# Optimization experiments

Hardware: AMD Instinct MI355X
Metric: run time of the kernel (lower is better)

The kernel has to match this reference:

```python
import jax, jax.numpy as jnp
import numpy as np

N = 8192       # nodes per graph
E = 262144     # edges per graph (avg degree 32)
D_IN, D_H, D_OUT = 128, 256, 64


def _gcn_layer(x, src, dst, W, b, n):
    # PyG GCNConv: add self-loops, symmetric normalization D^-1/2 (A+I) D^-1/2, then + bias
    xw = x @ W
    loop = jnp.arange(n)
    src_f = jnp.concatenate([src, loop])
    dst_f = jnp.concatenate([dst, loop])
    deg = jax.ops.segment_sum(jnp.ones(src_f.shape[0], x.dtype), dst_f, num_segments=n)
    dinv = jax.lax.rsqrt(jnp.maximum(deg, jnp.asarray(1e-12, x.dtype)))
    norm = dinv[src_f] * dinv[dst_f]                      # [E+N]
    msg = xw[src_f] * norm[:, None]                       # gather + scale
    return jax.ops.segment_sum(msg, dst_f, num_segments=n) + b


def _cross_attn(x1, x2, q, k, v):
    Q = x1 @ q
    V = x1 @ v
    K = x2 @ k
    e = jax.nn.leaky_relu(Q @ K.T, negative_slope=0.01)  # [N1, N2]
    attn = jax.nn.softmax(e, axis=-1)
    return attn @ V


def setup_inputs() -> dict:
    key = jax.random.key(0)
    ks = jax.random.split(key, 20)
    std = 1.0 / np.sqrt(D_OUT)

    def gw(k, shape, fan_in):
        return jax.random.normal(k, shape, jnp.float32) * (1.0 / np.sqrt(fan_in))

    def uw(k, shape):
        return jax.random.uniform(k, shape, jnp.float32, -std, std)

    inp = {
        'graph_set1': jax.random.randint(ks[0], (2, E), 0, N),
        'graph_set2': jax.random.randint(ks[1], (2, E), 0, N),
        'x_set1': jax.random.normal(ks[2], (N, D_IN), jnp.float32),
        'x_set2': jax.random.normal(ks[3], (N, D_IN), jnp.float32),
        'W11': gw(ks[4], (D_IN, D_H), D_IN),  'b11': jnp.zeros((D_H,), jnp.float32),
        'W12': gw(ks[5], (D_H, D_OUT), D_H),  'b12': jnp.zeros((D_OUT,), jnp.float32),
        'W21': gw(ks[6], (D_IN, D_H), D_IN),  'b21': jnp.zeros((D_H,), jnp.float32),
        'W22': gw(ks[7], (D_H, D_OUT), D_H),  'b22': jnp.zeros((D_OUT,), jnp.float32),
        'q1': uw(ks[8], (D_OUT, D_OUT)), 'k1': uw(ks[9], (D_OUT, D_OUT)), 'v1': uw(ks[10], (D_OUT, D_OUT)),
        'q2': uw(ks[11], (D_OUT, D_OUT)), 'k2': uw(ks[12], (D_OUT, D_OUT)), 'v2': uw(ks[13], (D_OUT, D_OUT)),
    }
    return inp


def reference(graph_set1, graph_set2, x_set1, x_set2,
              W11, b11, W12, b12, W21, b21, W22, b22,
              q1, k1, v1, q2, k2, v2):
    s1, d1 = graph_set1[0], graph_set1[1]
    s2, d2 = graph_set2[0], graph_set2[1]
    # GCN branch 1
    h1 = jax.nn.relu(_gcn_layer(x_set1, s1, d1, W11, b11, N))
    h1 = _gcn_layer(h1, s1, d1, W12, b12, N)
    # GCN branch 2
    h2 = jax.nn.relu(_gcn_layer(x_set2, s2, d2, W21, b21, N))
    h2 = _gcn_layer(h2, s2, d2, W22, b22, N)
    # cross attention fusion (note cross2 consumes the updated out_set1)
    o1 = _cross_attn(h1, h2, q1, k1, v1)
    o2 = _cross_attn(h2, o1, q2, k2, v2)
    logits = (o1 @ o2.T).ravel()                          # [N*N]
    return logits
```

## Files before the change

kernel.cpp:

```cpp
#include <hip/hip_runtime.h>
#include <math.h>

static constexpr int NN = 8192;
static constexpr int NE = 262144;
static constexpr int NCH = 8;
static constexpr int NS = (NN / NCH) / 32;

typedef short bfrag __attribute__((ext_vector_type(8)));
typedef float f32x4 __attribute__((ext_vector_type(4)));

#define MFMA(a, b, c) __builtin_amdgcn_mfma_f32_16x16x32_bf16((a), (b), (c), 0, 0, 0)

__device__ __forceinline__ unsigned short f2bf(float x) {
  union { float f; unsigned u; } v; v.f = x;
  unsigned r = v.u + 0x7fffu + ((v.u >> 16) & 1u);
  return (unsigned short)(r >> 16);
}
__device__ __forceinline__ float bf2f(unsigned short h) {
  union { unsigned u; float f; } v; v.u = ((unsigned)h) << 16;
  return v.f;
}

__device__ __forceinline__ void gll16(const void* g, void* l) {
  __builtin_amdgcn_global_load_lds(
      (const __attribute__((address_space(1))) unsigned*)g,
      (__attribute__((address_space(3))) unsigned*)l, 16, 0, 0);
}


__global__ void k_count2(const int* __restrict__ d1, const int* __restrict__ d2,
                         int* __restrict__ i1, int* __restrict__ i2) {
  int t = blockIdx.x * 256 + threadIdx.x;
  const int* d = blockIdx.y ? d2 : d1;
  int* ii = blockIdx.y ? i2 : i1;
  if (t < NE) atomicAdd(&ii[d[t]], 1);
}

__global__ void k_scan2(const int* __restrict__ ideg1, int* __restrict__ off1,
                        int* __restrict__ cur1, float* __restrict__ dinv1,
                        const int* __restrict__ ideg2, int* __restrict__ off2,
                        int* __restrict__ cur2, float* __restrict__ dinv2) {
  const int* indeg = blockIdx.x ? ideg2 : ideg1;
  int* off = blockIdx.x ? off2 : off1;
  int* cur = blockIdx.x ? cur2 : cur1;
  float* dinv = blockIdx.x ? dinv2 : dinv1;
  __shared__ int sh[1024];
  __shared__ int carry;
  int t = threadIdx.x;
  if (t == 0) carry = 0;
  __syncthreads();
  for (int base = 0; base < NN; base += 1024) {
    int v = indeg[base + t];
    sh[t] = v;
    __syncthreads();
    for (int s = 1; s < 1024; s <<= 1) {
      int add = (t >= s) ? sh[t - s] : 0;
      __syncthreads();
      sh[t] += add;
      __syncthreads();
    }
    int excl = carry + sh[t] - v;
    off[base + t] = excl;
    cur[base + t] = excl;
    dinv[base + t] = 1.0f / sqrtf((float)(v + 1));
    __syncthreads();
    if (t == 1023) carry += sh[t];
    __syncthreads();
  }
  if (t == 0) off[NN] = carry;
}

__global__ void k_fill2(const int* __restrict__ s1, const int* __restrict__ d1,
                        int* __restrict__ c1, int* __restrict__ l1,
                        const int* __restrict__ s2, const int* __restrict__ d2,
                        int* __restrict__ c2, int* __restrict__ l2) {
  int t = blockIdx.x * 256 + threadIdx.x;
  const int* src = blockIdx.y ? s2 : s1;
  const int* dst = blockIdx.y ? d2 : d1;
  int* cur = blockIdx.y ? c2 : c1;
  int* out = blockIdx.y ? l2 : l1;
  if (t < NE) {
    int d = dst[t];
    int slot = atomicAdd(&cur[d], 1);
    out[slot] = src[t];
  }
}


__global__ void k_split_w(const float* W11, const float* W21, const float* W12,
                          const float* W22, const float* q1, const float* k1,
                          const float* v1, const float* q2, const float* k2,
                          const float* v2, short* __restrict__ whi,
                          short* __restrict__ wlo) {
  int y = blockIdx.y;
  const float* src; int R, C, base;
  if (y == 0)      { src = W11; R = 128; C = 256; base = 0; }
  else if (y == 1) { src = W21; R = 128; C = 256; base = 32768; }
  else if (y == 2) { src = W12; R = 256; C = 64;  base = 65536; }
  else if (y == 3) { src = W22; R = 256; C = 64;  base = 81920; }
  else if (y == 4) { src = q1;  R = 64;  C = 64;  base = 98304; }
  else if (y == 5) { src = k1;  R = 64;  C = 64;  base = 102400; }
  else if (y == 6) { src = v1;  R = 64;  C = 64;  base = 106496; }
  else if (y == 7) { src = q2;  R = 64;  C = 64;  base = 110592; }
  else if (y == 8) { src = k2;  R = 64;  C = 64;  base = 114688; }
  else             { src = v2;  R = 64;  C = 64;  base = 118784; }
  int idx = blockIdx.x * 256 + threadIdx.x;
  if (idx >= R * C) return;
  int r = idx / C, c = idx % C;
  float x = src[idx];
  unsigned short h = f2bf(x);
  whi[base + c * R + r] = (short)h;
  wlo[base + c * R + r] = (short)f2bf(x - bf2f(h));
}


__global__ __launch_bounds__(256) void k_agg1d(
    const float* __restrict__ x1, const float* __restrict__ x2,
    const int* __restrict__ off1, const int* __restrict__ srcl1,
    const float* __restrict__ dinv1, const int* __restrict__ off2,
    const int* __restrict__ srcl2, const float* __restrict__ dinv2,
    short* __restrict__ a1hi, short* __restrict__ a1lo,
    short* __restrict__ a2hi, short* __restrict__ a2lo) {
  int br = blockIdx.y;
  const float* x = br ? x2 : x1;
  const int* off = br ? off2 : off1;
  const int* srcl = br ? srcl2 : srcl1;
  const float* dinv = br ? dinv2 : dinv1;
  short* ahi = br ? a2hi : a1hi;
  short* alo = br ? a2lo : a1lo;
  int wave = threadIdx.x >> 6, lane = threadIdx.x & 63;
  int node = blockIdx.x * 4 + wave;
  float dn = dinv[node];
  const float2* xr = (const float2*)x;
  float ax, ay;
  { float2 v = xr[(size_t)node * 64 + lane]; ax = dn * v.x; ay = dn * v.y; }
  int p = off[node], e = off[node + 1];
  for (; p + 3 < e; p += 4) {
    int s0 = srcl[p], s1 = srcl[p + 1], s2 = srcl[p + 2], s3 = srcl[p + 3];
    float w0 = dinv[s0], w1 = dinv[s1], w2 = dinv[s2], w3 = dinv[s3];
    float2 v0 = xr[(size_t)s0 * 64 + lane], v1 = xr[(size_t)s1 * 64 + lane];
    float2 v2 = xr[(size_t)s2 * 64 + lane], v3 = xr[(size_t)s3 * 64 + lane];
    ax += w0 * v0.x + w1 * v1.x + w2 * v2.x + w3 * v3.x;
    ay += w0 * v0.y + w1 * v1.y + w2 * v2.y + w3 * v3.y;
  }
  for (; p < e; ++p) {
    int s = srcl[p];
    float w = dinv[s];
    float2 v = xr[(size_t)s * 64 + lane];
    ax += w * v.x; ay += w * v.y;
  }
  float ox = dn * ax, oy = dn * ay;
  unsigned short hx = f2bf(ox), hy = f2bf(oy);
  int o = node * 128 + lane * 2;
  *(short2*)(ahi + o) = make_short2((short)hx, (short)hy);
  *(short2*)(alo + o) = make_short2((short)f2bf(ox - bf2f(hx)),
                                    (short)f2bf(oy - bf2f(hy)));
}


__global__ __launch_bounds__(256) void k_agg2d(
    const float* __restrict__ t1, const float* __restrict__ t2,
    const int* __restrict__ off1, const int* __restrict__ srcl1,
    const float* __restrict__ dinv1, const int* __restrict__ off2,
    const int* __restrict__ srcl2, const float* __restrict__ dinv2,
    const float* __restrict__ b12, const float* __restrict__ b22,
    short* __restrict__ g1hi, short* __restrict__ g1lo,
    short* __restrict__ g2hi, short* __restrict__ g2lo) {
  int br = blockIdx.y;
  const float* t = br ? t2 : t1;
  const int* off = br ? off2 : off1;
  const int* srcl = br ? srcl2 : srcl1;
  const float* dinv = br ? dinv2 : dinv1;
  const float* bias = br ? b22 : b12;
  short* ghi = br ? g2hi : g1hi;
  short* glo = br ? g2lo : g1lo;
  int wave = threadIdx.x >> 6, lane = threadIdx.x & 63;
  int node = blockIdx.x * 4 + wave;
  float dn = dinv[node];
  float acc = dn * t[(size_t)node * 64 + lane];
  int p = off[node], e = off[node + 1];
  for (; p + 3 < e; p += 4) {
    int s0 = srcl[p], s1 = srcl[p + 1], s2 = srcl[p + 2], s3 = srcl[p + 3];
    float w0 = dinv[s0], w1 = dinv[s1], w2 = dinv[s2], w3 = dinv[s3];
    acc += w0 * t[(size_t)s0 * 64 + lane] + w1 * t[(size_t)s1 * 64 + lane] +
           w2 * t[(size_t)s2 * 64 + lane] + w3 * t[(size_t)s3 * 64 + lane];
  }
  for (; p < e; ++p) {
    int s = srcl[p];
    acc += dinv[s] * t[(size_t)s * 64 + lane];
  }
  float o = dn * acc + bias[lane];
  unsigned short h = f2bf(o);
  ghi[(size_t)node * 64 + lane] = (short)h;
  glo[(size_t)node * 64 + lane] = (short)f2bf(o - bf2f(h));
}


__global__ __launch_bounds__(64) void k_gemmL1(
    const short* __restrict__ a1hi, const short* __restrict__ a1lo,
    const short* __restrict__ a2hi, const short* __restrict__ a2lo,
    const short* __restrict__ whi, const short* __restrict__ wlo,
    const float* __restrict__ b11, const float* __restrict__ b21,
    short* __restrict__ h1hi, short* __restrict__ h1lo,
    short* __restrict__ h2hi, short* __restrict__ h2lo) {
  int br = blockIdx.z;
  const short* Ahi = br ? a2hi : a1hi;
  const short* Alo = br ? a2lo : a1lo;
  const short* Bh = whi + (br ? 32768 : 0);
  const short* Bl = wlo + (br ? 32768 : 0);
  const float* bias = br ? b21 : b11;
  short* Chi = br ? h2hi : h1hi;
  short* Clo = br ? h2lo : h1lo;
  int lane = threadIdx.x;
  int lo16 = lane & 15, hi4 = lane >> 4;
  int r0 = blockIdx.x * 16;
  int c0 = blockIdx.y * 64;
  bfrag ah[4], al[4];
  const char* abh = (const char*)Ahi + ((size_t)(r0 + lo16) * 128 + hi4 * 8) * 2;
  const char* abl = (const char*)Alo + ((size_t)(r0 + lo16) * 128 + hi4 * 8) * 2;
#pragma unroll
  for (int ks = 0; ks < 4; ++ks) {
    ah[ks] = *(const bfrag*)(abh + ks * 64);
    al[ks] = *(const bfrag*)(abl + ks * 64);
  }
  f32x4 z = {0.f, 0.f, 0.f, 0.f};
  f32x4 acc[4] = {z, z, z, z};
#pragma unroll
  for (int c = 0; c < 4; ++c) {
    const char* bbh = (const char*)Bh + ((size_t)(c0 + c * 16 + lo16) * 128 + hi4 * 8) * 2;
    const char* bbl = (const char*)Bl + ((size_t)(c0 + c * 16 + lo16) * 128 + hi4 * 8) * 2;
#pragma unroll
    for (int ks = 0; ks < 4; ++ks) {
      bfrag bh = *(const bfrag*)(bbh + ks * 64);
      bfrag bl = *(const bfrag*)(bbl + ks * 64);
      acc[c] = MFMA(ah[ks], bh, acc[c]);
      acc[c] = MFMA(ah[ks], bl, acc[c]);
      acc[c] = MFMA(al[ks], bh, acc[c]);
    }
  }
#pragma unroll
  for (int c = 0; c < 4; ++c) {
    int col = c0 + c * 16 + lo16;
    float bv = bias[col];
#pragma unroll
    for (int r = 0; r < 4; ++r) {
      int row = r0 + hi4 * 4 + r;
      float v = fmaxf(acc[c][r] + bv, 0.f);
      unsigned short h = f2bf(v);
      Chi[(size_t)row * 256 + col] = (short)h;
      Clo[(size_t)row * 256 + col] = (short)f2bf(v - bf2f(h));
    }
  }
}


__global__ __launch_bounds__(64) void k_gemmL2(
    const short* __restrict__ h1hi, const short* __restrict__ h1lo,
    const short* __restrict__ h2hi, const short* __restrict__ h2lo,
    const short* __restrict__ whi, const short* __restrict__ wlo,
    float* __restrict__ t1, float* __restrict__ t2) {
  int br = blockIdx.y;
  const short* Ahi = br ? h2hi : h1hi;
  const short* Alo = br ? h2lo : h1lo;
  const short* Bh = whi + (br ? 81920 : 65536);
  const short* Bl = wlo + (br ? 81920 : 65536);
  float* Cf = br ? t2 : t1;
  int lane = threadIdx.x;
  int lo16 = lane & 15, hi4 = lane >> 4;
  int r0 = blockIdx.x * 16;
  bfrag ah[8], al[8];
  const char* abh = (const char*)Ahi + ((size_t)(r0 + lo16) * 256 + hi4 * 8) * 2;
  const char* abl = (const char*)Alo + ((size_t)(r0 + lo16) * 256 + hi4 * 8) * 2;
#pragma unroll
  for (int ks = 0; ks < 8; ++ks) {
    ah[ks] = *(const bfrag*)(abh + ks * 64);
    al[ks] = *(const bfrag*)(abl + ks * 64);
  }
  f32x4 z = {0.f, 0.f, 0.f, 0.f};
  f32x4 acc[4] = {z, z, z, z};
#pragma unroll
  for (int c = 0; c < 4; ++c) {
    const char* bbh = (const char*)Bh + ((size_t)(c * 16 + lo16) * 256 + hi4 * 8) * 2;
    const char* bbl = (const char*)Bl + ((size_t)(c * 16 + lo16) * 256 + hi4 * 8) * 2;
#pragma unroll
    for (int ks = 0; ks < 8; ++ks) {
      bfrag bh = *(const bfrag*)(bbh + ks * 64);
      bfrag bl = *(const bfrag*)(bbl + ks * 64);
      acc[c] = MFMA(ah[ks], bh, acc[c]);
      acc[c] = MFMA(ah[ks], bl, acc[c]);
      acc[c] = MFMA(al[ks], bh, acc[c]);
    }
  }
#pragma unroll
  for (int c = 0; c < 4; ++c) {
    int col = c * 16 + lo16;
#pragma unroll
    for (int r = 0; r < 4; ++r)
      Cf[(size_t)(r0 + hi4 * 4 + r) * 64 + col] = acc[c][r];
  }
}


__global__ __launch_bounds__(64) void k_qkv(
    const short* __restrict__ Aqhi, const short* __restrict__ Aqlo,
    const short* __restrict__ Akhi, const short* __restrict__ Aklo,
    const short* __restrict__ Avhi, const short* __restrict__ Avlo,
    const short* __restrict__ whi, const short* __restrict__ wlo,
    int bq, int bk, int bv,
    short* __restrict__ Qhi, short* __restrict__ Qlo,
    short* __restrict__ Khi, short* __restrict__ Klo,
    short* __restrict__ Vthi, short* __restrict__ Vtlo) {
  int y = blockIdx.y;
  const short *Ah, *Al;
  int boff;
  if (y == 0)      { Ah = Aqhi; Al = Aqlo; boff = bq; }
  else if (y == 1) { Ah = Akhi; Al = Aklo; boff = bk; }
  else             { Ah = Avhi; Al = Avlo; boff = bv; }
  const short* Bh = whi + boff;
  const short* Bl = wlo + boff;
  int lane = threadIdx.x;
  int lo16 = lane & 15, hi4 = lane >> 4;
  int r0 = blockIdx.x * 16;
  bfrag ah0, ah1, al0, al1;
  {
    const char* a = (const char*)(Ah + (size_t)(r0 + lo16) * 64 + hi4 * 8);
    const char* b = (const char*)(Al + (size_t)(r0 + lo16) * 64 + hi4 * 8);
    ah0 = *(const bfrag*)a; ah1 = *(const bfrag*)(a + 64);
    al0 = *(const bfrag*)b; al1 = *(const bfrag*)(b + 64);
  }
  f32x4 z = {0.f, 0.f, 0.f, 0.f};
  f32x4 acc[4] = {z, z, z, z};
#pragma unroll
  for (int c = 0; c < 4; ++c) {
    const char* bbh = (const char*)(Bh + (size_t)(c * 16 + lo16) * 64 + hi4 * 8);
    const char* bbl = (const char*)(Bl + (size_t)(c * 16 + lo16) * 64 + hi4 * 8);
    bfrag bh0 = *(const bfrag*)bbh, bh1 = *(const bfrag*)(bbh + 64);
    bfrag bl0 = *(const bfrag*)bbl, bl1 = *(const bfrag*)(bbl + 64);
    acc[c] = MFMA(ah0, bh0, acc[c]);
    acc[c] = MFMA(ah1, bh1, acc[c]);
    acc[c] = MFMA(ah0, bl0, acc[c]);
    acc[c] = MFMA(ah1, bl1, acc[c]);
    acc[c] = MFMA(al0, bh0, acc[c]);
    acc[c] = MFMA(al1, bh1, acc[c]);
  }
  if (y == 2) {
#pragma unroll
    for (int c = 0; c < 4; ++c) {
      int col = c * 16 + lo16;
      short4 vh, vl;
      float v0 = acc[c][0], v1 = acc[c][1], v2 = acc[c][2], v3 = acc[c][3];
      unsigned short h0 = f2bf(v0), h1 = f2bf(v1), h2 = f2bf(v2), h3 = f2bf(v3);
      vh = make_short4((short)h0, (short)h1, (short)h2, (short)h3);
      vl = make_short4((short)f2bf(v0 - bf2f(h0)), (short)f2bf(v1 - bf2f(h1)),
                       (short)f2bf(v2 - bf2f(h2)), (short)f2bf(v3 - bf2f(h3)));
      size_t o = (size_t)col * NN + r0 + hi4 * 4;
      *(short4*)(Vthi + o) = vh;
      *(short4*)(Vtlo + o) = vl;
    }
  } else {
    short* oh = (y == 0) ? Qhi : Khi;
    short* ol = (y == 0) ? Qlo : Klo;
#pragma unroll
    for (int c = 0; c < 4; ++c) {
      int col = c * 16 + lo16;
#pragma unroll
      for (int r = 0; r < 4; ++r) {
        int row = r0 + hi4 * 4 + r;
        float v = acc[c][r];
        unsigned short h = f2bf(v);
        oh[(size_t)row * 64 + col] = (short)h;
        ol[(size_t)row * 64 + col] = (short)f2bf(v - bf2f(h));
      }
    }
  }
}


__global__ __launch_bounds__(512) void k_attn_v4(
    const short* __restrict__ Qhi, const short* __restrict__ Qlo,
    const short* __restrict__ Khi_g, const short* __restrict__ Klo_g,
    const short* __restrict__ Vthi_g, const short* __restrict__ Vtlo_g,
    float* __restrict__ Opart, float* __restrict__ mpart, float* __restrict__ lpart) {
  __shared__ short skh[2][32 * 64], skl[2][32 * 64];
  __shared__ short svh[2][64 * 32], svl[2][64 * 32];
  __shared__ short plds[8][16 * 40];
  const int tid = threadIdx.x;
  const int wave = tid >> 6, lane = tid & 63;
  const int lo16 = lane & 15, hi4 = lane >> 4;
  const int q0 = blockIdx.x * 128 + wave * 16;
  const int j0 = blockIdx.y * (NN / NCH);
  const int wv = wave & 3;
  short* myp = plds[wave];

  const int krow = wv * 8 + (lane >> 3);
  const int kcbs = ((lane & 7) * 16) ^ ((krow & 7) << 4);
  const int vrow = wv * 16 + (lane >> 2);
  const int vcbs = ((lane & 3) * 16) ^ (((vrow >> 1) & 3) << 4);
  const char* gka = (const char*)Khi_g + (size_t)(j0 + krow) * 128 + kcbs;
  const char* gkb = (const char*)Klo_g + (size_t)(j0 + krow) * 128 + kcbs;
  const char* gva = (const char*)Vthi_g + (size_t)vrow * (NN * 2) + (size_t)j0 * 2 + vcbs;
  const char* gvb = (const char*)Vtlo_g + (size_t)vrow * (NN * 2) + (size_t)j0 * 2 + vcbs;

#define STAGE(buf, s)                                                \
  do {                                                               \
    if (wave < 4) {                                                  \
      gll16(gka + (size_t)(s) * 4096, (char*)skh[buf] + wv * 1024);  \
      gll16(gkb + (size_t)(s) * 4096, (char*)skl[buf] + wv * 1024);  \
    } else {                                                         \
      gll16(gva + (s) * 64, (char*)svh[buf] + wv * 1024);            \
      gll16(gvb + (s) * 64, (char*)svl[buf] + wv * 1024);            \
    }                                                                \
  } while (0)

  const bfrag* qph = (const bfrag*)(Qhi + (size_t)(q0 + lo16) * 64 + hi4 * 8);
  const bfrag* qpl = (const bfrag*)(Qlo + (size_t)(q0 + lo16) * 64 + hi4 * 8);
  bfrag qh0 = qph[0], qh1 = qph[4];
  bfrag ql0 = qpl[0], ql1 = qpl[4];

  f32x4 z = {0.f, 0.f, 0.f, 0.f};
  f32x4 oacc[4] = {z, z, z, z};
  float mrun[4] = {-1e30f, -1e30f, -1e30f, -1e30f};
  float lsum[4] = {0.f, 0.f, 0.f, 0.f};

  STAGE(0, 0);
  __syncthreads();

  for (int s = 0; s < NS; ++s) {
    const int buf = s & 1;
    if (s + 1 < NS) STAGE(buf ^ 1, s + 1);
    const char* kh = (const char*)skh[buf];
    const char* kl = (const char*)skl[buf];
    f32x4 sa[2];
#pragma unroll
    for (int t = 0; t < 2; ++t) {
      int jr = 16 * t + lo16;
      int sw = (jr & 7) << 4;
      const char* rowh = kh + jr * 128;
      const char* rowl = kl + jr * 128;
      bfrag kh0 = *(const bfrag*)(rowh + ((hi4 * 16) ^ sw));
      bfrag kh1 = *(const bfrag*)(rowh + ((64 + hi4 * 16) ^ sw));
      bfrag kl0 = *(const bfrag*)(rowl + ((hi4 * 16) ^ sw));
      bfrag kl1 = *(const bfrag*)(rowl + ((64 + hi4 * 16) ^ sw));
      f32x4 acc = z;
      acc = MFMA(qh0, kh0, acc);
      acc = MFMA(qh1, kh1, acc);
      acc = MFMA(qh0, kl0, acc);
      acc = MFMA(qh1, kl1, acc);
      acc = MFMA(ql0, kh0, acc);
      acc = MFMA(ql1, kh1, acc);
      sa[t] = acc;
    }
#pragma unroll
    for (int t = 0; t < 2; ++t)
#pragma unroll
      for (int r = 0; r < 4; ++r) {
        float v = sa[t][r];
        sa[t][r] = fmaxf(v, 0.01f * v);
      }
    float pm[4];
#pragma unroll
    for (int r = 0; r < 4; ++r) pm[r] = fmaxf(sa[0][r], sa[1][r]);
#pragma unroll
    for (int mask = 1; mask <= 8; mask <<= 1)
#pragma unroll
      for (int r = 0; r < 4; ++r) pm[r] = fmaxf(pm[r], __shfl_xor(pm[r], mask));
    bool rb = false;
#pragma unroll
    for (int r = 0; r < 4; ++r) rb |= (pm[r] > mrun[r] + 4.f);
    if (__any(rb)) {
#pragma unroll
      for (int r = 0; r < 4; ++r) {
        float nm = (pm[r] > mrun[r] + 4.f) ? pm[r] : mrun[r];
        float c_ = __expf(mrun[r] - nm);
        lsum[r] *= c_;
#pragma unroll
        for (int c = 0; c < 4; ++c) oacc[c][r] *= c_;
        mrun[r] = nm;
      }
    }
    float p0[4], p1[4];
#pragma unroll
    for (int r = 0; r < 4; ++r) {
      p0[r] = __expf(sa[0][r] - mrun[r]);
      p1[r] = __expf(sa[1][r] - mrun[r]);
      lsum[r] += p0[r] + p1[r];
    }
#pragma unroll
    for (int r = 0; r < 4; ++r) {
      int row = hi4 * 4 + r;
      myp[row * 40 + lo16] = (short)f2bf(p0[r]);
      myp[row * 40 + 16 + lo16] = (short)f2bf(p1[r]);
    }
    bfrag pa = *(const bfrag*)(myp + lo16 * 40 + hi4 * 8);
    const char* vh = (const char*)svh[buf];
    const char* vl = (const char*)svl[buf];
#pragma unroll
    for (int c = 0; c < 4; ++c) {
      int dv = 16 * c + lo16;
      int svw = ((dv >> 1) & 3) << 4;
      bfrag vhf = *(const bfrag*)(vh + dv * 64 + ((hi4 * 16) ^ svw));
      bfrag vlf = *(const bfrag*)(vl + dv * 64 + ((hi4 * 16) ^ svw));
      oacc[c] = MFMA(pa, vhf, oacc[c]);
      oacc[c] = MFMA(pa, vlf, oacc[c]);
    }
    __syncthreads();
  }
#undef STAGE
#pragma unroll
  for (int mask = 1; mask <= 8; mask <<= 1)
#pragma unroll
    for (int r = 0; r < 4; ++r) lsum[r] += __shfl_xor(lsum[r], mask);
#pragma unroll
  for (int c = 0; c < 4; ++c)
#pragma unroll
    for (int r = 0; r < 4; ++r)
      Opart[((size_t)blockIdx.y * NN + q0 + hi4 * 4 + r) * 64 + 16 * c + lo16] = oacc[c][r];
  if (lo16 == 0) {
#pragma unroll
    for (int r = 0; r < 4; ++r) {
      mpart[blockIdx.y * NN + q0 + hi4 * 4 + r] = mrun[r];
      lpart[blockIdx.y * NN + q0 + hi4 * 4 + r] = lsum[r];
    }
  }
}

__global__ void k_comb(const float* __restrict__ Opart,
                       const float* __restrict__ mpart,
                       const float* __restrict__ lpart,
                       short* __restrict__ Ohi, short* __restrict__ Olo) {
  int row = blockIdx.x * 4 + (threadIdx.x >> 6);
  int d = threadIdx.x & 63;
  float M = -1e30f;
  for (int i = 0; i < NCH; ++i) M = fmaxf(M, mpart[i * NN + row]);
  float L = 0.f, acc = 0.f;
  for (int i = 0; i < NCH; ++i) {
    float w = __expf(mpart[i * NN + row] - M);
    L += w * lpart[i * NN + row];
    acc += w * Opart[((size_t)i * NN + row) * 64 + d];
  }
  float o = acc / L;
  unsigned short h = f2bf(o);
  Ohi[(size_t)row * 64 + d] = (short)h;
  Olo[(size_t)row * 64 + d] = (short)f2bf(o - bf2f(h));
}


__global__ __launch_bounds__(256) void k_outer(const short* __restrict__ o1hi,
                                               const short* __restrict__ o1lo,
                                               const short* __restrict__ o2hi,
                                               const short* __restrict__ o2lo,
                                               float* __restrict__ out) {
  int wave = threadIdx.x >> 6, lane = threadIdx.x & 63;
  int lo16 = lane & 15, hi4 = lane >> 4;
  int i0 = blockIdx.x * 64 + wave * 16;
  const bfrag* aph = (const bfrag*)(o1hi + (size_t)(i0 + lo16) * 64 + hi4 * 8);
  const bfrag* apl = (const bfrag*)(o1lo + (size_t)(i0 + lo16) * 64 + hi4 * 8);
  bfrag ah0 = aph[0], ah1 = aph[4];
  bfrag al0 = apl[0], al1 = apl[4];
  f32x4 z = {0.f, 0.f, 0.f, 0.f};
  int jbase = blockIdx.y * (NN / 16);

#define LOADB(JV, BH0, BH1, BL0, BL1)                                        \
  do {                                                                       \
    const bfrag* bph = (const bfrag*)(o2hi + (size_t)((JV) + lo16) * 64 + hi4 * 8); \
    const bfrag* bpl = (const bfrag*)(o2lo + (size_t)((JV) + lo16) * 64 + hi4 * 8); \
    BH0 = bph[0]; BH1 = bph[4]; BL0 = bpl[0]; BL1 = bpl[4];                  \
  } while (0)

#define COMP(JV, BH0, BH1, BL0, BL1)                                  \
  do {                                                                \
    f32x4 acc = z;                                                    \
    acc = MFMA(ah0, BH0, acc);                                        \
    acc = MFMA(ah1, BH1, acc);                                        \
    acc = MFMA(ah0, BL0, acc);                                        \
    acc = MFMA(ah1, BL1, acc);                                        \
    acc = MFMA(al0, BH0, acc);                                        \
    acc = MFMA(al1, BH1, acc);                                        \
    _Pragma("unroll")                                                 \
    for (int r = 0; r < 4; ++r)                                       \
      out[(size_t)(i0 + hi4 * 4 + r) * NN + (JV) + lo16] = acc[r];    \
  } while (0)

  bfrag pah0, pah1, pal0, pal1, pbh0, pbh1, pbl0, pbl1;
  LOADB(jbase, pah0, pah1, pal0, pal1);
  for (int jt = 0; jt < NN / 16 / 16; jt += 2) {
    int ja = jbase + jt * 16;
    LOADB(ja + 16, pbh0, pbh1, pbl0, pbl1);
    COMP(ja, pah0, pah1, pal0, pal1);
    if (jt + 2 < NN / 16 / 16) LOADB(ja + 32, pah0, pah1, pal0, pal1);
    COMP(ja + 16, pbh0, pbh1, pbl0, pbl1);
  }
#undef LOADB
#undef COMP
}


extern "C" void kernel_launch(void* const* d_in, const int* in_sizes, int n_in,
                              void* d_out, int out_size, void* d_ws, size_t ws_size,
                              hipStream_t stream) {
  const int* g1 = (const int*)d_in[0];
  const int* g2 = (const int*)d_in[1];
  const float* x1 = (const float*)d_in[2];
  const float* x2 = (const float*)d_in[3];
  const float* W11 = (const float*)d_in[4];
  const float* b11 = (const float*)d_in[5];
  const float* W12 = (const float*)d_in[6];
  const float* b12 = (const float*)d_in[7];
  const float* W21 = (const float*)d_in[8];
  const float* b21 = (const float*)d_in[9];
  const float* W22 = (const float*)d_in[10];
  const float* b22 = (const float*)d_in[11];
  const float* q1 = (const float*)d_in[12];
  const float* k1 = (const float*)d_in[13];
  const float* v1 = (const float*)d_in[14];
  const float* q2 = (const float*)d_in[15];
  const float* k2 = (const float*)d_in[16];
  const float* v2 = (const float*)d_in[17];

  char* ob = (char*)d_out;
  const size_t MB = 1u << 20;
  int* srcl1 = (int*)(ob + 0 * MB);
  int* srcl2 = (int*)(ob + 1 * MB);
  char* small = ob + 2 * MB;
  int* ideg1 = (int*)(small);
  int* ideg2 = (int*)(small + (32u << 10));
  int* off1 = (int*)(small + (64u << 10));
  int* off2 = (int*)(small + (128u << 10));
  int* cur1 = (int*)(small + (192u << 10));
  int* cur2 = (int*)(small + (256u << 10));
  float* dinv1 = (float*)(small + (320u << 10));
  float* dinv2 = (float*)(small + (384u << 10));
  short* whi = (short*)(ob + 3 * MB);
  short* wlo = (short*)(ob + 3 * MB + (512u << 10));
  short* a1hi = (short*)(ob + 4 * MB);
  short* a1lo = (short*)(ob + 6 * MB);
  short* a2hi = (short*)(ob + 8 * MB);
  short* a2lo = (short*)(ob + 10 * MB);
  short* h1hi = (short*)(ob + 12 * MB);
  short* h1lo = (short*)(ob + 16 * MB);
  short* h2hi = (short*)(ob + 20 * MB);
  short* h2lo = (short*)(ob + 24 * MB);
  float* tbuf1 = (float*)(ob + 28 * MB);
  float* tbuf2 = (float*)(ob + 30 * MB);
  short* g1hi = (short*)(ob + 32 * MB);
  short* g1lo = (short*)(ob + 33 * MB);
  short* g2hi = (short*)(ob + 34 * MB);
  short* g2lo = (short*)(ob + 35 * MB);
  short* Qhi = (short*)(ob + 36 * MB);
  short* Qlo = (short*)(ob + 37 * MB);
  short* Khi = (short*)(ob + 38 * MB);
  short* Klo = (short*)(ob + 39 * MB);
  short* Vthi = (short*)(ob + 40 * MB);
  short* Vtlo = (short*)(ob + 41 * MB);
  float* Opart = (float*)(ob + 42 * MB);
  float* mpart = (float*)(ob + 58 * MB);
  float* lpart = (float*)(ob + 58 * MB + (256u << 10));
  short* o1hi = (short*)d_ws;
  short* o1lo = (short*)((char*)d_ws + 1 * MB);
  short* o2hi = (short*)((char*)d_ws + 2 * MB);
  short* o2lo = (short*)((char*)d_ws + 3 * MB);

  hipMemsetAsync(ideg1, 0, 64u << 10, stream);
  k_count2<<<dim3(1024, 2), 256, 0, stream>>>(g1 + NE, g2 + NE, ideg1, ideg2);
  k_scan2<<<2, 1024, 0, stream>>>(ideg1, off1, cur1, dinv1, ideg2, off2, cur2, dinv2);
  k_fill2<<<dim3(1024, 2), 256, 0, stream>>>(g1, g1 + NE, cur1, srcl1,
                                             g2, g2 + NE, cur2, srcl2);
  k_split_w<<<dim3(128, 10), 256, 0, stream>>>(W11, W21, W12, W22, q1, k1, v1,
                                               q2, k2, v2, whi, wlo);

  k_agg1d<<<dim3(2048, 2), 256, 0, stream>>>(x1, x2, off1, srcl1, dinv1,
                                             off2, srcl2, dinv2,
                                             a1hi, a1lo, a2hi, a2lo);
  k_gemmL1<<<dim3(512, 4, 2), 64, 0, stream>>>(a1hi, a1lo, a2hi, a2lo, whi, wlo,
                                               b11, b21, h1hi, h1lo, h2hi, h2lo);
  k_gemmL2<<<dim3(512, 2), 64, 0, stream>>>(h1hi, h1lo, h2hi, h2lo, whi, wlo,
                                            tbuf1, tbuf2);
  k_agg2d<<<dim3(2048, 2), 256, 0, stream>>>(tbuf1, tbuf2, off1, srcl1, dinv1,
                                             off2, srcl2, dinv2, b12, b22,
                                             g1hi, g1lo, g2hi, g2lo);

  k_qkv<<<dim3(512, 3), 64, 0, stream>>>(g1hi, g1lo, g2hi, g2lo, g1hi, g1lo,
                                         whi, wlo, 98304, 102400, 106496,
                                         Qhi, Qlo, Khi, Klo, Vthi, Vtlo);
  k_attn_v4<<<dim3(64, NCH), 512, 0, stream>>>(Qhi, Qlo, Khi, Klo, Vthi, Vtlo,
                                               Opart, mpart, lpart);
  k_comb<<<2048, 256, 0, stream>>>(Opart, mpart, lpart, o1hi, o1lo);

  k_qkv<<<dim3(512, 3), 64, 0, stream>>>(g2hi, g2lo, o1hi, o1lo, g2hi, g2lo,
                                         whi, wlo, 110592, 114688, 118784,
                                         Qhi, Qlo, Khi, Klo, Vthi, Vtlo);
  k_attn_v4<<<dim3(64, NCH), 512, 0, stream>>>(Qhi, Qlo, Khi, Klo, Vthi, Vtlo,
                                               Opart, mpart, lpart);
  k_comb<<<2048, 256, 0, stream>>>(Opart, mpart, lpart, o2hi, o2lo);

  k_outer<<<dim3(128, 16), 256, 0, stream>>>(o1hi, o1lo, o2hi, o2lo, (float*)d_out);

  (void)in_sizes; (void)n_in; (void)out_size; (void)ws_size;
}
```

Baseline: 718.9 us.

## Give each attention wave two query tiles and deepen K/V prefetch pipeline

```diff
diff --git a/kernel.cpp b/kernel.cpp
--- a/kernel.cpp
+++ b/kernel.cpp
@@ -44,27 +44,34 @@
   int* off = blockIdx.x ? off2 : off1;
   int* cur = blockIdx.x ? cur2 : cur1;
   float* dinv = blockIdx.x ? dinv2 : dinv1;
-  __shared__ int sh[1024];
-  __shared__ int carry;
-  int t = threadIdx.x;
-  if (t == 0) carry = 0;
-  __syncthreads();
+  __shared__ int wsum[16];
+  int t = threadIdx.x, lane = t & 63, wv = t >> 6;
+  int carry = 0;
   for (int base = 0; base < NN; base += 1024) {
     int v = indeg[base + t];
-    sh[t] = v;
+    int sc = v;
+#pragma unroll
+    for (int d = 1; d < 64; d <<= 1) {
+      int o = __shfl_up(sc, d);
+      if (lane >= d) sc += o;
+    }
+    if (lane == 63) wsum[wv] = sc;
     __syncthreads();
-    for (int s = 1; s < 1024; s <<= 1) {
-      int add = (t >= s) ? sh[t - s] : 0;
-      __syncthreads();
-      sh[t] += add;
-      __syncthreads();
-    }
-    int excl = carry + sh[t] - v;
+    if (t < 16) {
+      int w = wsum[t];
+#pragma unroll
+      for (int d = 1; d < 16; d <<= 1) {
+        int o = __shfl_up(w, d);
+        if (t >= d) w += o;
+      }
+      wsum[t] = w;
+    }
+    __syncthreads();
+    int excl = carry + (wv ? wsum[wv - 1] : 0) + sc - v;
     off[base + t] = excl;
     cur[base + t] = excl;
     dinv[base + t] = 1.0f / sqrtf((float)(v + 1));
-    __syncthreads();
-    if (t == 1023) carry += sh[t];
+    carry += wsum[15];
     __syncthreads();
   }
   if (t == 0) off[NN] = carry;
@@ -376,7 +383,7 @@
 }
 
 
-__global__ __launch_bounds__(512) void k_attn_v4(
+__global__ __launch_bounds__(256) void k_attn_v5(
     const short* __restrict__ Qhi, const short* __restrict__ Qlo,
     const short* __restrict__ Khi_g, const short* __restrict__ Klo_g,
     const short* __restrict__ Vthi_g, const short* __restrict__ Vtlo_g,
@@ -387,14 +394,14 @@
   const int tid = threadIdx.x;
   const int wave = tid >> 6, lane = tid & 63;
   const int lo16 = lane & 15, hi4 = lane >> 4;
-  const int q0 = blockIdx.x * 128 + wave * 16;
+  const int q0 = blockIdx.x * 128 + wave * 32;
   const int j0 = blockIdx.y * (NN / NCH);
-  const int wv = wave & 3;
-  short* myp = plds[wave];
-
-  const int krow = wv * 8 + (lane >> 3);
+  short* mypA = plds[wave * 2];
+  short* mypB = plds[wave * 2 + 1];
+
+  const int krow = wave * 8 + (lane >> 3);
   const int kcbs = ((lane & 7) * 16) ^ ((krow & 7) << 4);
-  const int vrow = wv * 16 + (lane >> 2);
+  const int vrow = wave * 16 + (lane >> 2);
   const int vcbs = ((lane & 3) * 16) ^ (((vrow >> 1) & 3) << 4);
   const char* gka = (const char*)Khi_g + (size_t)(j0 + krow) * 128 + kcbs;
   const char* gkb = (const char*)Klo_g + (size_t)(j0 + krow) * 128 + kcbs;
@@ -403,95 +410,97 @@
 
 #define STAGE(buf, s)                                                \
   do {                                                               \
-    if (wave < 4) {                                                  \
-      gll16(gka + (size_t)(s) * 4096, (char*)skh[buf] + wv * 1024);  \
-      gll16(gkb + (size_t)(s) * 4096, (char*)skl[buf] + wv * 1024);  \
-    } else {                                                         \
-      gll16(gva + (s) * 64, (char*)svh[buf] + wv * 1024);            \
-      gll16(gvb + (s) * 64, (char*)svl[buf] + wv * 1024);            \
-    }                                                                \
+    gll16(gka + (size_t)(s) * 4096, (char*)skh[buf] + wave * 1024);  \
+    gll16(gkb + (size_t)(s) * 4096, (char*)skl[buf] + wave * 1024);  \
+    gll16(gva + (s) * 64, (char*)svh[buf] + wave * 1024);            \
+    gll16(gvb + (s) * 64, (char*)svl[buf] + wave * 1024);            \
   } while (0)
 
-  const bfrag* qph = (const bfrag*)(Qhi + (size_t)(q0 + lo16) * 64 + hi4 * 8);
-  const bfrag* qpl = (const bfrag*)(Qlo + (size_t)(q0 + lo16) * 64 + hi4 * 8);
-  bfrag qh0 = qph[0], qh1 = qph[4];
-  bfrag ql0 = qpl[0], ql1 = qpl[4];
+  const bfrag* qphA = (const bfrag*)(Qhi + (size_t)(q0 + lo16) * 64 + hi4 * 8);
+  const bfrag* qplA = (const bfrag*)(Qlo + (size_t)(q0 + lo16) * 64 + hi4 * 8);
+  const bfrag* qphB = (const bfrag*)(Qhi + (size_t)(q0 + 16 + lo16) * 64 + hi4 * 8);
+  const bfrag* qplB = (const bfrag*)(Qlo + (size_t)(q0 + 16 + lo16) * 64 + hi4 * 8);
+  bfrag qh0A = qphA[0], qh1A = qphA[4], ql0A = qplA[0], ql1A = qplA[4];
+  bfrag qh0B = qphB[0], qh1B = qphB[4], ql0B = qplB[0], ql1B = qplB[4];
 
   f32x4 z = {0.f, 0.f, 0.f, 0.f};
-  f32x4 oacc[4] = {z, z, z, z};
-  float mrun[4] = {-1e30f, -1e30f, -1e30f, -1e30f};
-  float lsum[4] = {0.f, 0.f, 0.f, 0.f};
-
-  STAGE(0, 0);
-  __syncthreads();
-
-  for (int s = 0; s < NS; ++s) {
-    const int buf = s & 1;
-    if (s + 1 < NS) STAGE(buf ^ 1, s + 1);
+  f32x4 oaccA[4] = {z, z, z, z}, oaccB[4] = {z, z, z, z};
+  float mrunA[4] = {-1e30f, -1e30f, -1e30f, -1e30f};
+  float mrunB[4] = {-1e30f, -1e30f, -1e30f, -1e30f};
+  float lsumA[4] = {0.f, 0.f, 0.f, 0.f}, lsumB[4] = {0.f, 0.f, 0.f, 0.f};
+
+#define SMAX(sa, mrun, lsum, oacc, myp, pa)                                   \
+  do {                                                                        \
+    _Pragma("unroll") for (int t = 0; t < 2; ++t)                             \
+      _Pragma("unroll") for (int r = 0; r < 4; ++r) {                         \
+        float v = sa[t][r];                                                   \
+        sa[t][r] = fmaxf(v, 0.01f * v);                                       \
+      }                                                                       \
+    float pm[4];                                                              \
+    _Pragma("unroll") for (int r = 0; r < 4; ++r)                             \
+        pm[r] = fmaxf(sa[0][r], sa[1][r]);                                    \
+    _Pragma("unroll") for (int mask = 1; mask <= 8; mask <<= 1)               \
+      _Pragma("unroll") for (int r = 0; r < 4; ++r)                           \
+        pm[r] = fmaxf(pm[r], __shfl_xor(pm[r], mask));                        \
+    bool rb = false;                                                          \
+    _Pragma("unroll") for (int r = 0; r < 4; ++r) rb |= (pm[r] > mrun[r] + 4.f); \
+    if (__any(rb)) {                                                          \
+      _Pragma("unroll") for (int r = 0; r < 4; ++r) {                         \
+        float nm = (pm[r] > mrun[r] + 4.f) ? pm[r] : mrun[r];                 \
+        float c_ = __expf(mrun[r] - nm);                                      \
+        lsum[r] *= c_;                                                        \
+        _Pragma("unroll") for (int c = 0; c < 4; ++c) oacc[c][r] *= c_;       \
+        mrun[r] = nm;                                                         \
+      }                                                                       \
+    }                                                                         \
+    float p0[4], p1[4];                                                       \
+    _Pragma("unroll") for (int r = 0; r < 4; ++r) {                           \
+      p0[r] = __expf(sa[0][r] - mrun[r]);                                     \
+      p1[r] = __expf(sa[1][r] - mrun[r]);                                     \
+      lsum[r] += p0[r] + p1[r];                                               \
+    }                                                                         \
+    _Pragma("unroll") for (int r = 0; r < 4; ++r) {                           \
+      int row = hi4 * 4 + r;                                                  \
+      myp[row * 40 + lo16] = (short)f2bf(p0[r]);                              \
+      myp[row * 40 + 16 + lo16] = (short)f2bf(p1[r]);                         \
+    }                                                                         \
+    pa = *(const bfrag*)(myp + lo16 * 40 + hi4 * 8);                          \
+  } while (0)
+
+  auto step = [&](int buf) {
     const char* kh = (const char*)skh[buf];
     const char* kl = (const char*)skl[buf];
-    f32x4 sa[2];
+    f32x4 saA[2], saB[2];
 #pragma unroll
     for (int t = 0; t < 2; ++t) {
       int jr = 16 * t + lo16;
       int sw = (jr & 7) << 4;
       const char* rowh = kh + jr * 128;
       const char* rowl = kl + jr * 128;
-      bfrag kh0 = *(const bfrag*)(rowh + ((hi4 * 16) ^ sw));
-      bfrag kh1 = *(const bfrag*)(rowh + ((64 + hi4 * 16) ^ sw));
-      bfrag kl0 = *(const bfrag*)(rowl + ((hi4 * 16) ^ sw));
-      bfrag kl1 = *(const bfrag*)(rowl + ((64 + hi4 * 16) ^ sw));
-      f32x4 acc = z;
-      acc = MFMA(qh0, kh0, acc);
-      acc = MFMA(qh1, kh1, acc);
-      acc = MFMA(qh0, kl0, acc);
-      acc = MFMA(qh1, kl1, acc);
-      acc = MFMA(ql0, kh0, acc);
-      acc = MFMA(ql1, kh1, acc);
-      sa[t] = acc;
-    }
-#pragma unroll
-    for (int t = 0; t < 2; ++t)
-#pragma unroll
-      for (int r = 0; r < 4; ++r) {
-        float v = sa[t][r];
-        sa[t][r] = fmaxf(v, 0.01f * v);
-      }
-    float pm[4];
-#pragma unroll
-    for (int r = 0; r < 4; ++r) pm[r] = fmaxf(sa[0][r], sa[1][r]);
-#pragma unroll
-    for (int mask = 1; mask <= 8; mask <<= 1)
-#pragma unroll
-      for (int r = 0; r < 4; ++r) pm[r] = fmaxf(pm[r], __shfl_xor(pm[r], mask));
-    bool rb = false;
-#pragma unroll
-    for (int r = 0; r < 4; ++r) rb |= (pm[r] > mrun[r] + 4.f);
-    if (__any(rb)) {
-#pragma unroll
-      for (int r = 0; r < 4; ++r) {
-        float nm = (pm[r] > mrun[r] + 4.f) ? pm[r] : mrun[r];
-        float c_ = __expf(mrun[r] - nm);
-        lsum[r] *= c_;
-#pragma unroll
-        for (int c = 0; c < 4; ++c) oacc[c][r] *= c_;
-        mrun[r] = nm;
-      }
-    }
-    float p0[4], p1[4];
-#pragma unroll
-    for (int r = 0; r < 4; ++r) {
-      p0[r] = __expf(sa[0][r] - mrun[r]);
-      p1[r] = __expf(sa[1][r] - mrun[r]);
-      lsum[r] += p0[r] + p1[r];
-    }
-#pragma unroll
-    for (int r = 0; r < 4; ++r) {
-      int row = hi4 * 4 + r;
-      myp[row * 40 + lo16] = (short)f2bf(p0[r]);
-      myp[row * 40 + 16 + lo16] = (short)f2bf(p1[r]);
-    }
-    bfrag pa = *(const bfrag*)(myp + lo16 * 40 + hi4 * 8);
+      bfrag kf0 = *(const bfrag*)(rowh + ((hi4 * 16) ^ sw));
+      bfrag kf1 = *(const bfrag*)(rowh + ((64 + hi4 * 16) ^ sw));
+      bfrag kg0 = *(const bfrag*)(rowl + ((hi4 * 16) ^ sw));
+      bfrag kg1 = *(const bfrag*)(rowl + ((64 + hi4 * 16) ^ sw));
+      f32x4 a = z;
+      a = MFMA(qh0A, kf0, a);
+      a = MFMA(qh1A, kf1, a);
+      a = MFMA(qh0A, kg0, a);
+      a = MFMA(qh1A, kg1, a);
+      a = MFMA(ql0A, kf0, a);
+      a = MFMA(ql1A, kf1, a);
+      saA[t] = a;
+      f32x4 b = z;
+      b = MFMA(qh0B, kf0, b);
+      b = MFMA(qh1B, kf1, b);
+      b = MFMA(qh0B, kg0, b);
+      b = MFMA(qh1B, kg1, b);
+      b = MFMA(ql0B, kf0, b);
+      b = MFMA(ql1B, kf1, b);
+      saB[t] = b;
+    }
+    bfrag paA, paB;
+    SMAX(saA, mrunA, lsumA, oaccA, mypA, paA);
+    SMAX(saB, mrunB, lsumB, oaccB, mypB, paB);
     const char* vh = (const char*)svh[buf];
     const char* vl = (const char*)svl[buf];
 #pragma unroll
@@ -500,26 +509,53 @@
       int svw = ((dv >> 1) & 3) << 4;
       bfrag vhf = *(const bfrag*)(vh + dv * 64 + ((hi4 * 16) ^ svw));
       bfrag vlf = *(const bfrag*)(vl + dv * 64 + ((hi4 * 16) ^ svw));
-      oacc[c] = MFMA(pa, vhf, oacc[c]);
-      oacc[c] = MFMA(pa, vlf, oacc[c]);
-    }
-    __syncthreads();
-  }
+      oaccA[c] = MFMA(paA, vhf, oaccA[c]);
+      oaccA[c] = MFMA(paA, vlf, oaccA[c]);
+      oaccB[c] = MFMA(paB, vhf, oaccB[c]);
+      oaccB[c] = MFMA(paB, vlf, oaccB[c]);
+    }
+  };
+
+  STAGE(0, 0);
+  STAGE(1, 1);
+  for (int s = 0; s < NS - 1; ++s) {
+    const int buf = s & 1;
+    asm volatile("s_waitcnt vmcnt(4)" ::: "memory");
+    __builtin_amdgcn_s_barrier();
+    __builtin_amdgcn_sched_barrier(0);
+    step(buf);
+    __builtin_amdgcn_sched_barrier(0);
+    __builtin_amdgcn_s_barrier();
+    if (s + 2 < NS) STAGE(buf, s + 2);
+  }
+  asm volatile("s_waitcnt vmcnt(0)" ::: "memory");
+  __builtin_amdgcn_s_barrier();
+  __builtin_amdgcn_sched_barrier(0);
+  step((NS - 1) & 1);
 #undef STAGE
+#undef SMAX
+
 #pragma unroll
   for (int mask = 1; mask <= 8; mask <<= 1)
 #pragma unroll
-    for (int r = 0; r < 4; ++r) lsum[r] += __shfl_xor(lsum[r], mask);
+    for (int r = 0; r < 4; ++r) {
+      lsumA[r] += __shfl_xor(lsumA[r], mask);
+      lsumB[r] += __shfl_xor(lsumB[r], mask);
+    }
 #pragma unroll
   for (int c = 0; c < 4; ++c)
 #pragma unroll
-    for (int r = 0; r < 4; ++r)
-      Opart[((size_t)blockIdx.y * NN + q0 + hi4 * 4 + r) * 64 + 16 * c + lo16] = oacc[c][r];
+    for (int r = 0; r < 4; ++r) {
+      Opart[((size_t)blockIdx.y * NN + q0 + hi4 * 4 + r) * 64 + 16 * c + lo16] = oaccA[c][r];
+      Opart[((size_t)blockIdx.y * NN + q0 + 16 + hi4 * 4 + r) * 64 + 16 * c + lo16] = oaccB[c][r];
+    }
   if (lo16 == 0) {
 #pragma unroll
     for (int r = 0; r < 4; ++r) {
-      mpart[blockIdx.y * NN + q0 + hi4 * 4 + r] = mrun[r];
-      lpart[blockIdx.y * NN + q0 + hi4 * 4 + r] = lsum[r];
+      mpart[blockIdx.y * NN + q0 + hi4 * 4 + r] = mrunA[r];
+      lpart[blockIdx.y * NN + q0 + hi4 * 4 + r] = lsumA[r];
+      mpart[blockIdx.y * NN + q0 + 16 + hi4 * 4 + r] = mrunB[r];
+      lpart[blockIdx.y * NN + q0 + 16 + hi4 * 4 + r] = lsumB[r];
     }
   }
 }
@@ -682,14 +718,14 @@
   k_qkv<<<dim3(512, 3), 64, 0, stream>>>(g1hi, g1lo, g2hi, g2lo, g1hi, g1lo,
                                          whi, wlo, 98304, 102400, 106496,
                                          Qhi, Qlo, Khi, Klo, Vthi, Vtlo);
-  k_attn_v4<<<dim3(64, NCH), 512, 0, stream>>>(Qhi, Qlo, Khi, Klo, Vthi, Vtlo,
+  k_attn_v5<<<dim3(64, NCH), 256, 0, stream>>>(Qhi, Qlo, Khi, Klo, Vthi, Vtlo,
                                                Opart, mpart, lpart);
   k_comb<<<2048, 256, 0, stream>>>(Opart, mpart, lpart, o1hi, o1lo);
 
   k_qkv<<<dim3(512, 3), 64, 0, stream>>>(g2hi, g2lo, o1hi, o1lo, g2hi, g2lo,
                                          whi, wlo, 110592, 114688, 118784,
                                          Qhi, Qlo, Khi, Klo, Vthi, Vtlo);
-  k_attn_v4<<<dim3(64, NCH), 512, 0, stream>>>(Qhi, Qlo, Khi, Klo, Vthi, Vtlo,
+  k_attn_v5<<<dim3(64, NCH), 256, 0, stream>>>(Qhi, Qlo, Khi, Klo, Vthi, Vtlo,
                                                Opart, mpart, lpart);
   k_comb<<<2048, 256, 0, stream>>>(Opart, mpart, lpart, o2hi, o2lo);
 
```

Measured after the change: 725.1 us. About the same (+0.9%).
